# Optimization experiments

Hardware: AMD Instinct MI355X
Metric: run time of the kernel (lower is better)

Reference implementation:

```python
import jax, jax.numpy as jnp
import numpy as np

B = 32768
H = 320          # pred_hidden
V = 34           # num_classes
BLANK = V - 1    # padding_idx for embedding


def setup_inputs() -> dict:
    key = jax.random.key(0)
    ks = jax.random.split(key, 12)
    s = 0.05
    embed_W = jax.random.normal(ks[0], (V, H), jnp.float32) * s
    embed_W = embed_W.at[BLANK].set(0.0)  # padding_idx row is zeros in torch
    return {
        "x": jax.random.randint(ks[1], (B,), 0, V, jnp.int32),
        "enc_proj_line": jax.random.normal(ks[2], (B, H), jnp.float32),
        "h": jax.random.normal(ks[3], (1, B, H), jnp.float32),
        "c": jax.random.normal(ks[4], (1, B, H), jnp.float32),
        "embed_W": embed_W,
        "W_ih": jax.random.normal(ks[5], (4 * H, H), jnp.float32) * s,
        "W_hh": jax.random.normal(ks[6], (4 * H, H), jnp.float32) * s,
        "b_ih": jax.random.normal(ks[7], (4 * H,), jnp.float32) * s,
        "b_hh": jax.random.normal(ks[8], (4 * H,), jnp.float32) * s,
        "pred_W": jax.random.normal(ks[9], (H, H), jnp.float32) * s,
        "pred_b": jnp.zeros((H,), jnp.float32),
        "joint_W": jax.random.normal(ks[10], (V, H), jnp.float32) * s,
        "joint_b": jnp.zeros((V,), jnp.float32),
    }


def reference(x, enc_proj_line, h, c, embed_W, W_ih, W_hh, b_ih, b_hh,
              pred_W, pred_b, joint_W, joint_b):
    # embedding lookup: [B, H]
    emb = embed_W[x]
    # single-timestep LSTM cell (torch gate order: i, f, g, o)
    gates = emb @ W_ih.T + b_ih + h[0] @ W_hh.T + b_hh  # [B, 4H]
    i, f, g, o = jnp.split(gates, 4, axis=-1)
    i = jax.nn.sigmoid(i)
    f = jax.nn.sigmoid(f)
    g = jnp.tanh(g)
    o = jax.nn.sigmoid(o)
    c_new = f * c[0] + i * g                 # [B, H]
    h_new = o * jnp.tanh(c_new)              # [B, H] == g[0] (lstm output)
    # pred projection + joint
    pred_proj = h_new @ pred_W.T + pred_b    # [B, H]
    joint_out = (enc_proj_line + pred_proj) @ joint_W.T + joint_b  # [B, V]
    dec = jnp.argmax(joint_out, axis=-1)
    return dec, h_new[None], c_new[None]
```

## Files before the change

kernel.cpp:

```cpp
#include <hip/hip_runtime.h>
#include <math.h>

#define NB 32768
#define H 320
#define V 34
#define N4 1280
#define BM 128
#define BN 128
#define KSTEPS 10
#define NWG ((NB / BM) * (N4 / BN))

typedef _Float16 f16;
typedef f16 f16x4 __attribute__((ext_vector_type(4)));
typedef f16 f16x8 __attribute__((ext_vector_type(8)));
typedef float f32x4 __attribute__((ext_vector_type(4)));

#define WS_GTP 0
#define WS_JB2 54400
#define WS_B_BYTE 217744
#define BT_COUNT (N4 * H)
#define WS_JP_BYTE 1856144
#define JP_COUNT (48 * 640)
#define WS_AT_BYTE 1979136
#define AT_COUNT (NB * H)

#define JBM 64
#define JBK 32
#define JKSTEPS 20

#define PREP_P4 1280
#define PREP_P2 50
#define PREP_P0 170
#define PREP_P3 120
#define PREP_NWG (PREP_P4 + PREP_P2 + PREP_P0 + PREP_P3 + 1)

__device__ __forceinline__ float sigf(float x) {
    return 1.0f / (1.0f + __expf(-x));
}
__device__ __forceinline__ float tanh_fast(float x) {
    return 1.0f - 2.0f / (1.0f + __expf(2.0f * x));
}

typedef const __attribute__((address_space(1))) unsigned int* gas_t;
typedef __attribute__((address_space(3))) unsigned int* las_t;

__device__ __forceinline__ void split8(const float* e, f16x8& p1, f16x8& p2) {
    #pragma unroll
    for (int j = 0; j < 8; ++j) {
        f16 a = (f16)e[j];
        p1[j] = a;
        p2[j] = (f16)((e[j] - (float)a) * 2048.0f);
    }
}

__device__ __forceinline__ void split8_res(const float* e, f16x8& p1, f16x8& p2) {
    #pragma unroll
    for (int j = 0; j < 8; ++j) {
        f16 a = (f16)e[j];
        p1[j] = a;
        p2[j] = (f16)(e[j] - (float)a);
    }
}

__global__ void prep(const float* __restrict__ embed_W,
                     const float* __restrict__ W_ih,
                     const float* __restrict__ b_ih,
                     const float* __restrict__ b_hh,
                     const float* __restrict__ pred_W,
                     const float* __restrict__ pred_b,
                     const float* __restrict__ joint_W,
                     const float* __restrict__ joint_b,
                     const float* __restrict__ W_hh,
                     const float* __restrict__ h_in,
                     float* __restrict__ ws) {
    const int bid = blockIdx.x;
    const int t = threadIdx.x;
    if (bid < PREP_P4) {
        int id = bid * 256 + t;
        int ks = id >> 15, m = id & 32767;
        const float* src = h_in + (size_t)m * H + ks * 32;
        f16* at1 = (f16*)((char*)ws + WS_AT_BYTE);
        f16* at2 = at1 + AT_COUNT;
        size_t tbase = ((size_t)(m >> 7) * KSTEPS + ks) * 4096
                       + ((m & 127) >> 4) * 512 + (m & 15) * 8;
        #pragma unroll
        for (int g = 0; g < 4; ++g) {
            float4 v0 = *(const float4*)(src + g * 8);
            float4 v1 = *(const float4*)(src + g * 8 + 4);
            float e[8] = {v0.x, v0.y, v0.z, v0.w, v1.x, v1.y, v1.z, v1.w};
            f16x8 p1, p2;
            split8_res(e, p1, p2);
            *(f16x8*)(at1 + tbase + g * 128) = p1;
            *(f16x8*)(at2 + tbase + g * 128) = p2;
        }
    } else if (bid < PREP_P4 + PREP_P2) {
        int id = (bid - PREP_P4) * 256 + t;
        int ks = id / 1280, n = id - ks * 1280;
        int orig = (n & 3) * H + (n >> 2);
        const float* src = W_hh + (size_t)orig * H + ks * 32;
        f16* bt1 = (f16*)((char*)ws + WS_B_BYTE);
        f16* bt2 = bt1 + BT_COUNT;
        size_t tbase = ((size_t)(n >> 7) * KSTEPS + ks) * 4096
                       + ((n & 127) >> 4) * 512 + (n & 15) * 8;
        #pragma unroll
        for (int g = 0; g < 4; ++g) {
            float4 v0 = *(const float4*)(src + g * 8);
            float4 v1 = *(const float4*)(src + g * 8 + 4);
            float e[8] = {v0.x, v0.y, v0.z, v0.w, v1.x, v1.y, v1.z, v1.w};
            f16x8 p1, p2;
            split8(e, p1, p2);
            *(f16x8*)(bt1 + tbase + g * 128) = p1;
            *(f16x8*)(bt2 + tbase + g * 128) = p2;
        }
    } else if (bid < PREP_P4 + PREP_P2 + PREP_P0) {
        int id = (bid - PREP_P4 - PREP_P2) * 256 + t;
        int v = id / N4, n = id % N4;
        int orig = (n & 3) * H + (n >> 2);
        float acc = b_ih[orig] + b_hh[orig];
        const float* e = embed_W + (size_t)v * H;
        const float* w = W_ih + (size_t)orig * H;
        for (int k = 0; k < H; k += 4) {
            float4 e4 = *(const float4*)(e + k);
            float4 w4 = *(const float4*)(w + k);
            acc = fmaf(e4.x, w4.x, acc);
            acc = fmaf(e4.y, w4.y, acc);
            acc = fmaf(e4.z, w4.z, acc);
            acc = fmaf(e4.w, w4.w, acc);
        }
        ws[WS_GTP + id] = acc;
    } else if (bid < PREP_P4 + PREP_P2 + PREP_P0 + PREP_P3) {
        int id = (bid - PREP_P4 - PREP_P2 - PREP_P0) * 256 + t;
        int n = id / 640, k = id % 640;
        float wv = 0.0f;
        if (n < V) {
            if (k < H) {
                wv = joint_W[(size_t)n * H + k];
            } else {
                float acc = 0.0f;
                const float* jw = joint_W + (size_t)n * H;
                for (int j = 0; j < H; ++j)
                    acc = fmaf(jw[j], pred_W[(size_t)j * H + (k - H)], acc);
                wv = acc;
            }
        }
        f16 w1 = (f16)wv;
        f16 w2 = (f16)((wv - (float)w1) * 2048.0f);
        int kk = k & 31;
        int off = (k >> 5) * 1536 + (n >> 4) * 512 + (kk >> 3) * 128
                  + (n & 15) * 8 + (kk & 7);
        f16* jp1 = (f16*)((char*)ws + WS_JP_BYTE);
        jp1[off] = w1;
        jp1[JP_COUNT + off] = w2;
    } else {
        if (t < V) {
            float acc = joint_b[t];
            const float* jw = joint_W + (size_t)t * H;
            for (int j = 0; j < H; ++j)
                acc = fmaf(jw[j], pred_b[j], acc);
            ws[WS_JB2 + t] = acc;
        }
    }
}

__launch_bounds__(512, 4)
__global__ void lstm_gemm_fast(const int* __restrict__ x,
                               const float* __restrict__ c_in,
                               const float* __restrict__ ws,
                               float* __restrict__ out) {
    __shared__ __align__(16) char smem[32768];
    const int tid = threadIdx.x, lane = tid & 63, w = tid >> 6;

    int l = (blockIdx.x & 7) * (NWG / 8) + (blockIdx.x >> 3);
    const int mb = l / (N4 / BN);
    const int nb = l % (N4 / BN);
    const int m0 = mb * BM, n0 = nb * BN;

    const f16* At1 = (const f16*)((const char*)ws + WS_AT_BYTE);
    const f16* At2 = At1 + AT_COUNT;
    const f16* Bt1 = (const f16*)((const char*)ws + WS_B_BYTE);
    const f16* Bt2 = Bt1 + BT_COUNT;
    const float* gtp = ws + WS_GTP;
    float* hn_out = out + NB;
    float* cn_out = out + NB + (size_t)NB * H;

    const int wr = w >> 2;
    const int wc = w & 3;
    const int asub = wr * 4;
    const int bsub = wc * 2;
    const int lo = lane * 8;

    auto stageB = [&](int ks, int parity) {
        const f16* srcp = (w < 4) ? Bt1 : Bt2;
        const f16* src = srcp + (size_t)(nb * KSTEPS + ks) * 4096 + (w & 3) * 1024;
        char* dst = smem + parity * 16384 + ((w < 4) ? 0 : 8192) + (w & 3) * 2048;
        #pragma unroll
        for (int i = 0; i < 2; ++i) {
            __builtin_amdgcn_global_load_lds(
                (gas_t)(const void*)(src + i * 512 + lane * 8),
                (las_t)(void*)(dst + i * 1024), 16, 0, 0);
        }
    };

    f32x4 acc[4][2];
    #pragma unroll
    for (int i = 0; i < 4; ++i) {
        acc[i][0] = (f32x4){0.f, 0.f, 0.f, 0.f};
        acc[i][1] = (f32x4){0.f, 0.f, 0.f, 0.f};
    }

    f16x8 a1r[4], a2r[4];

    stageB(0, 0);
    __builtin_amdgcn_sched_barrier(0);
    {
        const f16* a1b = At1 + (size_t)(mb * KSTEPS) * 4096;
        const f16* a2b = At2 + (size_t)(mb * KSTEPS) * 4096;
        #pragma unroll
        for (int mi = 0; mi < 4; ++mi) {
            a1r[mi] = *(const f16x8*)(a1b + (asub + mi) * 512 + lo);
            a2r[mi] = *(const f16x8*)(a2b + (asub + mi) * 512 + lo);
        }
    }
    __builtin_amdgcn_sched_barrier(0);
    const int hk0 = n0 >> 2;
    float cpre[8];
    #pragma unroll
    for (int j = 0; j < 8; ++j)
        cpre[j] = c_in[(size_t)(m0 + j * 16 + (tid >> 5)) * H + hk0 + (tid & 31)];
    __builtin_amdgcn_sched_barrier(0);
    asm volatile("s_waitcnt vmcnt(16)" ::: "memory");
    __builtin_amdgcn_sched_barrier(0);
    __builtin_amdgcn_s_barrier();

    #pragma unroll
    for (int t = 0; t < KSTEPS; ++t) {
        const int par = t & 1;
        if (t < KSTEPS - 1) {
            stageB(t + 1, par ^ 1);
            __builtin_amdgcn_sched_barrier(0);
        }
        const f16* B1 = (const f16*)(smem + par * 16384);
        const f16* B2 = B1 + 4096;

        f16x8 b1[2], b2[2];
        #pragma unroll
        for (int nj = 0; nj < 2; ++nj) {
            b1[nj] = *(const f16x8*)(B1 + (bsub + nj) * 512 + lo);
            b2[nj] = *(const f16x8*)(B2 + (bsub + nj) * 512 + lo);
        }

        __builtin_amdgcn_s_setprio(1);
        #pragma unroll
        for (int mi = 0; mi < 4; ++mi)
            #pragma unroll
            for (int nj = 0; nj < 2; ++nj)
                acc[mi][nj] = __builtin_amdgcn_mfma_f32_16x16x32_f16(
                    a1r[mi], b1[nj], acc[mi][nj], 0, 0, 0);
        __builtin_amdgcn_s_setprio(0);
        #pragma unroll
        for (int mi = 0; mi < 4; ++mi)
            #pragma unroll
            for (int j = 0; j < 8; ++j)
                a1r[mi][j] = a1r[mi][j] * (f16)0.00048828125f;
        __builtin_amdgcn_s_setprio(1);
        #pragma unroll
        for (int mi = 0; mi < 4; ++mi)
            #pragma unroll
            for (int nj = 0; nj < 2; ++nj)
                acc[mi][nj] = __builtin_amdgcn_mfma_f32_16x16x32_f16(
                    a1r[mi], b2[nj], acc[mi][nj], 0, 0, 0);
        __builtin_amdgcn_s_setprio(0);
        if (t < KSTEPS - 1) {
            const f16* a1b = At1 + (size_t)(mb * KSTEPS + t + 1) * 4096;
            #pragma unroll
            for (int mi = 0; mi < 4; ++mi)
                a1r[mi] = *(const f16x8*)(a1b + (asub + mi) * 512 + lo);
            __builtin_amdgcn_sched_barrier(0);
        }
        __builtin_amdgcn_s_setprio(1);
        #pragma unroll
        for (int mi = 0; mi < 4; ++mi)
            #pragma unroll
            for (int nj = 0; nj < 2; ++nj)
                acc[mi][nj] = __builtin_amdgcn_mfma_f32_16x16x32_f16(
                    a2r[mi], b1[nj], acc[mi][nj], 0, 0, 0);
        __builtin_amdgcn_s_setprio(0);
        if (t < KSTEPS - 1) {
            const f16* a2b = At2 + (size_t)(mb * KSTEPS + t + 1) * 4096;
            #pragma unroll
            for (int mi = 0; mi < 4; ++mi)
                a2r[mi] = *(const f16x8*)(a2b + (asub + mi) * 512 + lo);
            __builtin_amdgcn_sched_barrier(0);
            asm volatile("s_waitcnt vmcnt(8)" ::: "memory");
            __builtin_amdgcn_sched_barrier(0);
            __builtin_amdgcn_s_barrier();
        } else {
            __syncthreads();
        }
    }

    float* gates = (float*)smem;
    #pragma unroll
    for (int hf = 0; hf < 2; ++hf) {
        if (wr == hf) {
            #pragma unroll
            for (int mi = 0; mi < 4; ++mi)
                #pragma unroll
                for (int nj = 0; nj < 2; ++nj) {
                    f32x4 v = acc[mi][nj];
                    int n = wc * 32 + nj * 16 + (lane & 15);
                    int lr0 = mi * 16 + (lane >> 4) * 4;
                    #pragma unroll
                    for (int q = 0; q < 4; ++q) {
                        int lr = lr0 + q;
                        gates[lr * 128 + (n ^ ((lr & 7) << 2))] = v[q];
                    }
                }
        }
        __syncthreads();
        int xv[4];
        #pragma unroll
        for (int it = 0; it < 4; ++it)
            xv[it] = x[m0 + hf * 64 + it * 16 + (tid >> 5)];
        float4 b4[4];
        #pragma unroll
        for (int it = 0; it < 4; ++it)
            b4[it] = *(const float4*)(gtp + (size_t)xv[it] * N4 + n0 + (tid & 31) * 4);
        #pragma unroll
        for (int it = 0; it < 4; ++it) {
            int ml = it * 16 + (tid >> 5), hkl = tid & 31;
            int k0s = (ml & 7) << 2;
            f32x4 g4 = *(const f32x4*)&gates[ml * 128 + ((hkl * 4) ^ k0s)];
            int m = m0 + hf * 64 + ml;
            int hk = hk0 + hkl;
            float ig = sigf(g4[0] + b4[it].x);
            float fg = sigf(g4[1] + b4[it].y);
            float gg = tanh_fast(g4[2] + b4[it].z);
            float og = sigf(g4[3] + b4[it].w);
            float cn = fmaf(fg, cpre[hf * 4 + it], ig * gg);
            float hn = og * tanh_fast(cn);
            hn_out[(size_t)m * H + hk] = hn;
            cn_out[(size_t)m * H + hk] = cn;
        }
        if (hf == 0) __syncthreads();
    }
}

__launch_bounds__(256, 2)
__global__ void joint_argmax(const float* __restrict__ enc,
                             const float* __restrict__ ws,
                             float* __restrict__ out) {
    __shared__ __align__(16) char smem[28672];
    const int tid = threadIdx.x, lane = tid & 63, w = tid >> 6;
    const int m0 = blockIdx.x * JBM;

    const f16* Jp1 = (const f16*)((const char*)ws + WS_JP_BYTE);
    const f16* Jp2 = Jp1 + JP_COUNT;
    const float* hn = out + NB;
    const float* jb2 = ws + WS_JB2;

    f16* base = (f16*)smem;

    f32x4 accM[3], accC[3];
    #pragma unroll
    for (int j = 0; j < 3; ++j) {
        accM[j] = (f32x4){0.f, 0.f, 0.f, 0.f};
        accC[j] = (f32x4){0.f, 0.f, 0.f, 0.f};
    }

    auto stage = [&](int t, f16* A1, f16* A2, f16* B1, f16* B2) {
        const float* srcp = (t < 10) ? enc : hn;
        const int koff = (t % 10) * JBK;
        int row = (tid >> 6) * 16 + (tid & 15);
        int k0 = ((tid & 63) >> 4) * 8;
        const float* sp = srcp + (size_t)(m0 + row) * H + koff + k0;
        float4 v0 = *(const float4*)sp;
        float4 v1 = *(const float4*)(sp + 4);
        float e[8] = {v0.x, v0.y, v0.z, v0.w, v1.x, v1.y, v1.z, v1.w};
        f16x8 p1, p2;
        split8(e, p1, p2);
        *(f16x8*)(A1 + tid * 8) = p1;
        *(f16x8*)(A2 + tid * 8) = p2;
        if (tid < 192) {
            *(int4*)(B1 + tid * 8) = *(const int4*)(Jp1 + t * 1536 + tid * 8);
            *(int4*)(B2 + tid * 8) = *(const int4*)(Jp2 + t * 1536 + tid * 8);
        }
    };

    stage(0, base, base + 2048, base + 4096, base + 5632);
    __syncthreads();

    const int lo = lane * 8;
    int cur = 0;
    for (int t = 0; t < JKSTEPS; ++t) {
        if (t < JKSTEPS - 1) {
            f16* nb_ = base + (cur ^ 1) * 7168;
            stage(t + 1, nb_, nb_ + 2048, nb_ + 4096, nb_ + 5632);
        }
        f16* A1 = base + cur * 7168;
        f16* A2 = A1 + 2048;
        f16* B1 = A1 + 4096;
        f16* B2 = A1 + 5632;

        f16x8 a1 = *(const f16x8*)(A1 + w * 512 + lo);
        f16x8 a2 = *(const f16x8*)(A2 + w * 512 + lo);
        f16x8 b1[3], b2[3];
        #pragma unroll
        for (int nj = 0; nj < 3; ++nj) {
            b1[nj] = *(const f16x8*)(B1 + nj * 512 + lo);
            b2[nj] = *(const f16x8*)(B2 + nj * 512 + lo);
        }
        #pragma unroll
        for (int nj = 0; nj < 3; ++nj) {
            accM[nj] = __builtin_amdgcn_mfma_f32_16x16x32_f16(a1, b1[nj], accM[nj], 0, 0, 0);
            accC[nj] = __builtin_amdgcn_mfma_f32_16x16x32_f16(a1, b2[nj], accC[nj], 0, 0, 0);
            accC[nj] = __builtin_amdgcn_mfma_f32_16x16x32_f16(a2, b1[nj], accC[nj], 0, 0, 0);
        }
        __syncthreads();
        cur ^= 1;
    }

    float* lg = (float*)smem;
    const int wm = w * 16;
    #pragma unroll
    for (int nj = 0; nj < 3; ++nj) {
        int n = nj * 16 + (lane & 15);
        int mr = wm + (lane >> 4) * 4;
        #pragma unroll
        for (int q = 0; q < 4; ++q)
            lg[(mr + q) * 49 + n] = fmaf(accC[nj][q], 1.0f / 2048.0f, accM[nj][q]);
    }
    __syncthreads();

    if (tid < JBM) {
        const float* row = lg + tid * 49;
        float best = row[0] + jb2[0];
        int bi = 0;
        #pragma unroll
        for (int v = 1; v < V; ++v) {
            float t2 = row[v] + jb2[v];
            if (t2 > best) { best = t2; bi = v; }
        }
        out[m0 + tid] = (float)bi;
    }
}

extern "C" void kernel_launch(void* const* d_in, const int* in_sizes, int n_in,
                              void* d_out, int out_size, void* d_ws, size_t ws_size,
                              hipStream_t stream) {
    const int*   x       = (const int*)  d_in[0];
    const float* enc     = (const float*)d_in[1];
    const float* h       = (const float*)d_in[2];
    const float* c       = (const float*)d_in[3];
    const float* embed_W = (const float*)d_in[4];
    const float* W_ih    = (const float*)d_in[5];
    const float* W_hh    = (const float*)d_in[6];
    const float* b_ih    = (const float*)d_in[7];
    const float* b_hh    = (const float*)d_in[8];
    const float* pred_W  = (const float*)d_in[9];
    const float* pred_b  = (const float*)d_in[10];
    const float* joint_W = (const float*)d_in[11];
    const float* joint_b = (const float*)d_in[12];
    float* out = (float*)d_out;
    float* ws  = (float*)d_ws;

    prep<<<PREP_NWG, 256, 0, stream>>>(embed_W, W_ih, b_ih, b_hh,
                                       pred_W, pred_b, joint_W, joint_b,
                                       W_hh, h, ws);
    lstm_gemm_fast<<<NWG, 512, 0, stream>>>(x, c, ws, out);
    joint_argmax<<<NB / JBM, 256, 0, stream>>>(enc, ws, out);
}
```

Before: 170.7 us.

## Halve LSTM GEMM tile width, load B directly to registers, per-wave epilogue

The LSTM gate GEMM tile goes from 128x128 with 512 threads to 128x64 with 256 threads, doubling the workgroup count. The B operand is now loaded straight from global memory into double-buffered registers, replacing the async global-to-LDS staging and the block barriers in the K loop. The epilogue has each wave write its accumulators to a private padded LDS patch, so no block-wide sync is needed. This removes barrier and LDS traffic in the main loop, at the cost of more global and L2 reads, because A tiles are re-read by twice as many workgroups.

```diff
diff --git a/kernel.cpp b/kernel.cpp
--- a/kernel.cpp
+++ b/kernel.cpp
@@ -6,9 +6,10 @@
 #define V 34
 #define N4 1280
 #define BM 128
-#define BN 128
+#define BN 64
+#define NBQ (N4 / BN)
 #define KSTEPS 10
-#define NWG ((NB / BM) * (N4 / BN))
+#define NWG ((NB / BM) * NBQ)
 
 typedef _Float16 f16;
 typedef f16 f16x4 __attribute__((ext_vector_type(4)));
@@ -40,9 +41,6 @@
 __device__ __forceinline__ float tanh_fast(float x) {
     return 1.0f - 2.0f / (1.0f + __expf(2.0f * x));
 }
-
-typedef const __attribute__((address_space(1))) unsigned int* gas_t;
-typedef __attribute__((address_space(3))) unsigned int* las_t;
 
 __device__ __forceinline__ void split8(const float* e, f16x8& p1, f16x8& p2) {
     #pragma unroll
@@ -162,18 +160,19 @@
     }
 }
 
-__launch_bounds__(512, 4)
+__launch_bounds__(256, 4)
 __global__ void lstm_gemm_fast(const int* __restrict__ x,
                                const float* __restrict__ c_in,
                                const float* __restrict__ ws,
                                float* __restrict__ out) {
-    __shared__ __align__(16) char smem[32768];
+    __shared__ __align__(16) float patch[4][64 * 36];
     const int tid = threadIdx.x, lane = tid & 63, w = tid >> 6;
 
     int l = (blockIdx.x & 7) * (NWG / 8) + (blockIdx.x >> 3);
-    const int mb = l / (N4 / BN);
-    const int nb = l % (N4 / BN);
-    const int m0 = mb * BM, n0 = nb * BN;
+    const int mb = l / NBQ;
+    const int nbq = l % NBQ;
+    const int m0 = mb * BM, n0 = nbq * BN;
+    const int wr = w >> 1, wc = w & 1;
 
     const f16* At1 = (const f16*)((const char*)ws + WS_AT_BYTE);
     const f16* At2 = At1 + AT_COUNT;
@@ -183,23 +182,15 @@
     float* hn_out = out + NB;
     float* cn_out = out + NB + (size_t)NB * H;
 
-    const int wr = w >> 2;
-    const int wc = w & 3;
+    const int lo = lane * 8;
+    const int pb = nbq >> 1;
+    const int bsub = (nbq & 1) * 4 + wc * 2;
     const int asub = wr * 4;
-    const int bsub = wc * 2;
-    const int lo = lane * 8;
-
-    auto stageB = [&](int ks, int parity) {
-        const f16* srcp = (w < 4) ? Bt1 : Bt2;
-        const f16* src = srcp + (size_t)(nb * KSTEPS + ks) * 4096 + (w & 3) * 1024;
-        char* dst = smem + parity * 16384 + ((w < 4) ? 0 : 8192) + (w & 3) * 2048;
-        #pragma unroll
-        for (int i = 0; i < 2; ++i) {
-            __builtin_amdgcn_global_load_lds(
-                (gas_t)(const void*)(src + i * 512 + lane * 8),
-                (las_t)(void*)(dst + i * 1024), 16, 0, 0);
-        }
-    };
+
+    const f16* a1base = At1 + (size_t)mb * KSTEPS * 4096 + asub * 512 + lo;
+    const f16* a2base = At2 + (size_t)mb * KSTEPS * 4096 + asub * 512 + lo;
+    const f16* b1base = Bt1 + (size_t)pb * KSTEPS * 4096 + bsub * 512 + lo;
+    const f16* b2base = Bt2 + (size_t)pb * KSTEPS * 4096 + bsub * 512 + lo;
 
     f32x4 acc[4][2];
     #pragma unroll
@@ -208,73 +199,62 @@
         acc[i][1] = (f32x4){0.f, 0.f, 0.f, 0.f};
     }
 
-    f16x8 a1r[4], a2r[4];
-
-    stageB(0, 0);
+    f16x8 a1[4], a2[4], b1[2][2], b2[2];
+
+    #pragma unroll
+    for (int mi = 0; mi < 4; ++mi) a1[mi] = *(const f16x8*)(a1base + mi * 512);
+    #pragma unroll
+    for (int nj = 0; nj < 2; ++nj) b1[0][nj] = *(const f16x8*)(b1base + nj * 512);
+    #pragma unroll
+    for (int nj = 0; nj < 2; ++nj) b2[nj] = *(const f16x8*)(b2base + nj * 512);
+    #pragma unroll
+    for (int mi = 0; mi < 4; ++mi) a2[mi] = *(const f16x8*)(a2base + mi * 512);
     __builtin_amdgcn_sched_barrier(0);
-    {
-        const f16* a1b = At1 + (size_t)(mb * KSTEPS) * 4096;
-        const f16* a2b = At2 + (size_t)(mb * KSTEPS) * 4096;
-        #pragma unroll
-        for (int mi = 0; mi < 4; ++mi) {
-            a1r[mi] = *(const f16x8*)(a1b + (asub + mi) * 512 + lo);
-            a2r[mi] = *(const f16x8*)(a2b + (asub + mi) * 512 + lo);
-        }
-    }
+    const int hk0c = (n0 >> 2) + wc * 8;
+    float cpre[8];
+    #pragma unroll
+    for (int i = 0; i < 8; ++i)
+        cpre[i] = c_in[(size_t)(m0 + wr * 64 + i * 8 + (lane >> 3)) * H
+                       + hk0c + (lane & 7)];
     __builtin_amdgcn_sched_barrier(0);
-    const int hk0 = n0 >> 2;
-    float cpre[8];
-    #pragma unroll
-    for (int j = 0; j < 8; ++j)
-        cpre[j] = c_in[(size_t)(m0 + j * 16 + (tid >> 5)) * H + hk0 + (tid & 31)];
-    __builtin_amdgcn_sched_barrier(0);
-    asm volatile("s_waitcnt vmcnt(16)" ::: "memory");
-    __builtin_amdgcn_sched_barrier(0);
-    __builtin_amdgcn_s_barrier();
 
     #pragma unroll
     for (int t = 0; t < KSTEPS; ++t) {
-        const int par = t & 1;
+        const int cb = t & 1;
         if (t < KSTEPS - 1) {
-            stageB(t + 1, par ^ 1);
+            #pragma unroll
+            for (int nj = 0; nj < 2; ++nj)
+                b1[cb ^ 1][nj] = *(const f16x8*)(b1base + (t + 1) * 4096 + nj * 512);
             __builtin_amdgcn_sched_barrier(0);
         }
-        const f16* B1 = (const f16*)(smem + par * 16384);
-        const f16* B2 = B1 + 4096;
-
-        f16x8 b1[2], b2[2];
-        #pragma unroll
-        for (int nj = 0; nj < 2; ++nj) {
-            b1[nj] = *(const f16x8*)(B1 + (bsub + nj) * 512 + lo);
-            b2[nj] = *(const f16x8*)(B2 + (bsub + nj) * 512 + lo);
-        }
-
         __builtin_amdgcn_s_setprio(1);
         #pragma unroll
         for (int mi = 0; mi < 4; ++mi)
             #pragma unroll
             for (int nj = 0; nj < 2; ++nj)
                 acc[mi][nj] = __builtin_amdgcn_mfma_f32_16x16x32_f16(
-                    a1r[mi], b1[nj], acc[mi][nj], 0, 0, 0);
+                    a1[mi], b1[cb][nj], acc[mi][nj], 0, 0, 0);
         __builtin_amdgcn_s_setprio(0);
         #pragma unroll
         for (int mi = 0; mi < 4; ++mi)
             #pragma unroll
             for (int j = 0; j < 8; ++j)
-                a1r[mi][j] = a1r[mi][j] * (f16)0.00048828125f;
+                a1[mi][j] = a1[mi][j] * (f16)0.00048828125f;
         __builtin_amdgcn_s_setprio(1);
         #pragma unroll
         for (int mi = 0; mi < 4; ++mi)
             #pragma unroll
             for (int nj = 0; nj < 2; ++nj)
                 acc[mi][nj] = __builtin_amdgcn_mfma_f32_16x16x32_f16(
-                    a1r[mi], b2[nj], acc[mi][nj], 0, 0, 0);
+                    a1[mi], b2[nj], acc[mi][nj], 0, 0, 0);
         __builtin_amdgcn_s_setprio(0);
         if (t < KSTEPS - 1) {
-            const f16* a1b = At1 + (size_t)(mb * KSTEPS + t + 1) * 4096;
             #pragma unroll
             for (int mi = 0; mi < 4; ++mi)
-                a1r[mi] = *(const f16x8*)(a1b + (asub + mi) * 512 + lo);
+                a1[mi] = *(const f16x8*)(a1base + (t + 1) * 4096 + mi * 512);
+            #pragma unroll
+            for (int nj = 0; nj < 2; ++nj)
+                b2[nj] = *(const f16x8*)(b2base + (t + 1) * 4096 + nj * 512);
             __builtin_amdgcn_sched_barrier(0);
         }
         __builtin_amdgcn_s_setprio(1);
@@ -283,66 +263,47 @@
             #pragma unroll
             for (int nj = 0; nj < 2; ++nj)
                 acc[mi][nj] = __builtin_amdgcn_mfma_f32_16x16x32_f16(
-                    a2r[mi], b1[nj], acc[mi][nj], 0, 0, 0);
+                    a2[mi], b1[cb][nj], acc[mi][nj], 0, 0, 0);
         __builtin_amdgcn_s_setprio(0);
         if (t < KSTEPS - 1) {
-            const f16* a2b = At2 + (size_t)(mb * KSTEPS + t + 1) * 4096;
             #pragma unroll
             for (int mi = 0; mi < 4; ++mi)
-                a2r[mi] = *(const f16x8*)(a2b + (asub + mi) * 512 + lo);
+                a2[mi] = *(const f16x8*)(a2base + (t + 1) * 4096 + mi * 512);
             __builtin_amdgcn_sched_barrier(0);
-            asm volatile("s_waitcnt vmcnt(8)" ::: "memory");
-            __builtin_amdgcn_sched_barrier(0);
-            __builtin_amdgcn_s_barrier();
-        } else {
-            __syncthreads();
-        }
-    }
-
-    float* gates = (float*)smem;
-    #pragma unroll
-    for (int hf = 0; hf < 2; ++hf) {
-        if (wr == hf) {
-            #pragma unroll
-            for (int mi = 0; mi < 4; ++mi)
-                #pragma unroll
-                for (int nj = 0; nj < 2; ++nj) {
-                    f32x4 v = acc[mi][nj];
-                    int n = wc * 32 + nj * 16 + (lane & 15);
-                    int lr0 = mi * 16 + (lane >> 4) * 4;
-                    #pragma unroll
-                    for (int q = 0; q < 4; ++q) {
-                        int lr = lr0 + q;
-                        gates[lr * 128 + (n ^ ((lr & 7) << 2))] = v[q];
-                    }
-                }
-        }
-        __syncthreads();
-        int xv[4];
-        #pragma unroll
-        for (int it = 0; it < 4; ++it)
-            xv[it] = x[m0 + hf * 64 + it * 16 + (tid >> 5)];
-        float4 b4[4];
-        #pragma unroll
-        for (int it = 0; it < 4; ++it)
-            b4[it] = *(const float4*)(gtp + (size_t)xv[it] * N4 + n0 + (tid & 31) * 4);
-        #pragma unroll
-        for (int it = 0; it < 4; ++it) {
-            int ml = it * 16 + (tid >> 5), hkl = tid & 31;
-            int k0s = (ml & 7) << 2;
-            f32x4 g4 = *(const f32x4*)&gates[ml * 128 + ((hkl * 4) ^ k0s)];
-            int m = m0 + hf * 64 + ml;
-            int hk = hk0 + hkl;
-            float ig = sigf(g4[0] + b4[it].x);
-            float fg = sigf(g4[1] + b4[it].y);
-            float gg = tanh_fast(g4[2] + b4[it].z);
-            float og = sigf(g4[3] + b4[it].w);
-            float cn = fmaf(fg, cpre[hf * 4 + it], ig * gg);
-            float hn = og * tanh_fast(cn);
-            hn_out[(size_t)m * H + hk] = hn;
-            cn_out[(size_t)m * H + hk] = cn;
-        }
-        if (hf == 0) __syncthreads();
+        }
+    }
+
+    float* myp = patch[w];
+    #pragma unroll
+    for (int mi = 0; mi < 4; ++mi)
+        #pragma unroll
+        for (int nj = 0; nj < 2; ++nj) {
+            int col = nj * 16 + (lane & 15);
+            int r0 = mi * 16 + (lane >> 4) * 4;
+            #pragma unroll
+            for (int q = 0; q < 4; ++q)
+                myp[(r0 + q) * 36 + col] = acc[mi][nj][q];
+        }
+    asm volatile("s_waitcnt lgkmcnt(0)" ::: "memory");
+    __builtin_amdgcn_sched_barrier(0);
+
+    const int hkl = lane & 7;
+    #pragma unroll
+    for (int i = 0; i < 8; ++i) {
+        int ml = i * 8 + (lane >> 3);
+        f32x4 g4 = *(const f32x4*)&myp[ml * 36 + hkl * 4];
+        int m = m0 + wr * 64 + ml;
+        int hk = hk0c + hkl;
+        int xv = x[m];
+        float4 b4 = *(const float4*)(gtp + (size_t)xv * N4 + hk * 4);
+        float ig = sigf(g4[0] + b4.x);
+        float fg = sigf(g4[1] + b4.y);
+        float gg = tanh_fast(g4[2] + b4.z);
+        float og = sigf(g4[3] + b4.w);
+        float cn = fmaf(fg, cpre[i], ig * gg);
+        float hn = og * tanh_fast(cn);
+        hn_out[(size_t)m * H + hk] = hn;
+        cn_out[(size_t)m * H + hk] = cn;
     }
 }
 
@@ -467,6 +428,6 @@
     prep<<<PREP_NWG, 256, 0, stream>>>(embed_W, W_ih, b_ih, b_hh,
                                        pred_W, pred_b, joint_W, joint_b,
                                        W_hh, h, ws);
-    lstm_gemm_fast<<<NWG, 512, 0, stream>>>(x, c, ws, out);
+    lstm_gemm_fast<<<NWG, 256, 0, stream>>>(x, c, ws, out);
     joint_argmax<<<NB / JBM, 256, 0, stream>>>(enc, ws, out);
 }
```

Result: no change. 170.4 us (-0.2%).
